# Performance work log

Measured on AMD Instinct MI355X. Metric: run time of the kernel, lower is better.

## Reference

```python
import jax, jax.numpy as jnp
import numpy as np
import math

B, N, D_IN, D_V, H, D_FF = 8, 2048, 256, 256, 8, 512
HD = D_V // H  # head dim = 32
EPS = 1e-5


def layernorm(x, g, b):
    mu = jnp.mean(x, axis=-1, keepdims=True)
    var = jnp.mean(jnp.square(x - mu), axis=-1, keepdims=True)
    return (x - mu) * jax.lax.rsqrt(var + EPS) * g + b


def setup_inputs() -> dict:
    key = jax.random.key(0)
    ks = jax.random.split(key, 12)
    s = 1.0 / math.sqrt(D_IN)
    return {
        "x": jax.random.normal(ks[0], (B, N, D_IN), jnp.float32),
        "y": jax.random.normal(ks[1], (B, N, D_IN), jnp.float32),
        "Wq": jax.random.normal(ks[2], (D_IN, D_V), jnp.float32) * s,
        "bq": jnp.zeros((D_V,), jnp.float32),
        "Wk": jax.random.normal(ks[3], (D_IN, D_V), jnp.float32) * s,
        "bk": jnp.zeros((D_V,), jnp.float32),
        "Wv": jax.random.normal(ks[4], (D_IN, D_V), jnp.float32) * s,
        "bv": jnp.zeros((D_V,), jnp.float32),
        "W1": jax.random.normal(ks[5], (D_V, D_FF), jnp.float32) * s,
        "b1": jnp.zeros((D_FF,), jnp.float32),
        "W2": jax.random.normal(ks[6], (D_FF, D_V), jnp.float32) * (1.0 / math.sqrt(D_FF)),
        "b2": jnp.zeros((D_V,), jnp.float32),
        "ln0_g": jnp.ones((D_IN,), jnp.float32),
        "ln0_b": jnp.zeros((D_IN,), jnp.float32),
        "ln1_g": jnp.ones((D_V,), jnp.float32),
        "ln1_b": jnp.zeros((D_V,), jnp.float32),
    }


def reference(x, y, Wq, bq, Wk, bk, Wv, bv, W1, b1, W2, b2, ln0_g, ln0_b, ln1_g, ln1_b):
    xn = layernorm(x, ln0_g, ln0_b)                      # ln0 on queries
    Q = (xn @ Wq + bq).reshape(B, N, H, HD)              # [B,Nq,H,hd]
    K = (y @ Wk + bk).reshape(B, N, H, HD)
    V = (y @ Wv + bv).reshape(B, N, H, HD)
    # NOTE: faithful scale = 1/sqrt(dim_V) (full model dim), not head dim
    S = jnp.einsum("bqhd,bkhd->bhqk", Q, K) / math.sqrt(D_V)
    A = jax.nn.softmax(S, axis=-1)
    O = Q + jnp.einsum("bhqk,bkhd->bqhd", A, V)          # per-head residual Q_ + A
    O = O.reshape(B, N, D_V)
    On = layernorm(O, ln1_g, ln1_b)
    ff = jax.nn.gelu(On @ W1 + b1, approximate=False) @ W2 + b2
    return O + ff
```

## Files before the change

kernel.cpp:

```cpp
#include <hip/hip_runtime.h>
#include <math.h>

#define RTOT 16384
#define NSEQ 2048
#define NHEAD 8
#define HDIM 32
#define QSCALE 0.09017132252479462f

typedef __attribute__((ext_vector_type(8))) short short8;
typedef __attribute__((ext_vector_type(4))) float f32x4;

#define GLOBAL_AS(p) ((__attribute__((address_space(1))) void*)(p))
#define LDS_AS(p) ((__attribute__((address_space(3))) void*)(p))

__device__ __forceinline__ unsigned pack_bf16(float a, float b) {
  unsigned ua = __float_as_uint(a) + 0x8000u;
  unsigned ub = __float_as_uint(b) + 0x8000u;
  return (ua >> 16) | (ub & 0xffff0000u);
}
__device__ __forceinline__ ushort bf16_1(float a) {
  return (ushort)((__float_as_uint(a) + 0x8000u) >> 16);
}

__global__ __launch_bounds__(256) void stage0_kernel(
    const float* __restrict__ x, const float* __restrict__ y,
    const float* __restrict__ Wq, const float* __restrict__ Wk,
    const float* __restrict__ Wv, const float* __restrict__ W1,
    const float* __restrict__ W2, const float* __restrict__ ln0g,
    const float* __restrict__ ln0b, ushort* __restrict__ Wqt,
    ushort* __restrict__ Wkt, ushort* __restrict__ Wvt,
    ushort* __restrict__ W1t, ushort* __restrict__ W2t,
    ushort* __restrict__ yh, ushort* __restrict__ xh) {
  const int bid = blockIdx.x;
  const int t = threadIdx.x;
  if (bid < 112) {
    const float* W;
    ushort* Wt;
    int K, N, tile;
    if (bid < 16) { W = Wq; Wt = Wqt; K = 256; N = 256; tile = bid; }
    else if (bid < 32) { W = Wk; Wt = Wkt; K = 256; N = 256; tile = bid - 16; }
    else if (bid < 48) { W = Wv; Wt = Wvt; K = 256; N = 256; tile = bid - 32; }
    else if (bid < 80) { W = W1; Wt = W1t; K = 256; N = 512; tile = bid - 48; }
    else { W = W2; Wt = W2t; K = 512; N = 256; tile = bid - 80; }
    const int tn = N >> 6;
    const int k0 = (tile / tn) << 6, n0 = (tile % tn) << 6;
    __shared__ float T[64][65];
#pragma unroll
    for (int i = 0; i < 16; ++i) {
      const int idx = t + i * 256;
      const int r = idx >> 6, c = idx & 63;
      T[r][c] = W[(size_t)(k0 + r) * N + n0 + c];
    }
    __syncthreads();
#pragma unroll
    for (int i = 0; i < 16; ++i) {
      const int idx = t + i * 256;
      const int r = idx >> 6, c = idx & 63;
      Wt[(size_t)(n0 + r) * K + k0 + c] = bf16_1(T[c][r]);
    }
  } else if (bid < 4208) {
    const size_t i = ((size_t)(bid - 112) * 256 + t) * 4;
    const float4 v = *(const float4*)&y[i];
    uint2 pk;
    pk.x = pack_bf16(v.x, v.y);
    pk.y = pack_bf16(v.z, v.w);
    *(uint2*)&yh[i] = pk;
  } else {
    const int lane = t & 63, wave = t >> 6;
    const size_t row = (size_t)(bid - 4208) * 4 + wave;
    const float* xr = x + row * 256;
    float4 v = *(const float4*)&xr[lane * 4];
    float s = v.x + v.y + v.z + v.w;
#pragma unroll
    for (int m = 1; m < 64; m <<= 1) s += __shfl_xor(s, m, 64);
    const float mu = s * (1.0f / 256.0f);
    const float dx = v.x - mu, dy = v.y - mu, dz = v.z - mu, dw = v.w - mu;
    float ss = dx * dx + dy * dy + dz * dz + dw * dw;
#pragma unroll
    for (int m = 1; m < 64; m <<= 1) ss += __shfl_xor(ss, m, 64);
    const float rstd = rsqrtf(ss * (1.0f / 256.0f) + 1e-5f);
    const float4 gv = *(const float4*)&ln0g[lane * 4];
    const float4 bv = *(const float4*)&ln0b[lane * 4];
    uint2 pk;
    pk.x = pack_bf16(dx * rstd * gv.x + bv.x, dy * rstd * gv.y + bv.y);
    pk.y = pack_bf16(dz * rstd * gv.z + bv.z, dw * rstd * gv.w + bv.w);
    *(uint2*)&xh[row * 256 + lane * 4] = pk;
  }
}

__global__ __launch_bounds__(256) void ln_kernel(
    const float* __restrict__ X, const float* __restrict__ g,
    const float* __restrict__ bt, ushort* __restrict__ Yh) {
  const int lane = threadIdx.x & 63;
  const int wave = threadIdx.x >> 6;
  const size_t row = (size_t)blockIdx.x * 4 + wave;
  const float* xr = X + row * 256;
  float4 v = *(const float4*)&xr[lane * 4];
  float s = v.x + v.y + v.z + v.w;
#pragma unroll
  for (int m = 1; m < 64; m <<= 1) s += __shfl_xor(s, m, 64);
  const float mu = s * (1.0f / 256.0f);
  const float dx = v.x - mu, dy = v.y - mu, dz = v.z - mu, dw = v.w - mu;
  float ss = dx * dx + dy * dy + dz * dz + dw * dw;
#pragma unroll
  for (int m = 1; m < 64; m <<= 1) ss += __shfl_xor(ss, m, 64);
  const float rstd = rsqrtf(ss * (1.0f / 256.0f) + 1e-5f);
  const float4 gv = *(const float4*)&g[lane * 4];
  const float4 bv = *(const float4*)&bt[lane * 4];
  uint2 pk;
  pk.x = pack_bf16(dx * rstd * gv.x + bv.x, dy * rstd * gv.y + bv.y);
  pk.y = pack_bf16(dz * rstd * gv.z + bv.z, dw * rstd * gv.w + bv.w);
  *(uint2*)&Yh[row * 256 + lane * 4] = pk;
}

__global__ __launch_bounds__(256) void qkv_kernel(
    const ushort* __restrict__ xh, const ushort* __restrict__ yh,
    const ushort* __restrict__ Wqt, const ushort* __restrict__ Wkt,
    const ushort* __restrict__ Wvt, const float* __restrict__ bq,
    const float* __restrict__ bk, const float* __restrict__ bv,
    float* __restrict__ Qf, ushort* __restrict__ Qh,
    ushort* __restrict__ Kh, ushort* __restrict__ VhT) {
  __shared__ union UU {
    struct { ushort As[128 * 32]; ushort Bs[64 * 32]; } s;
    ushort Ct[64 * 136];
  } u;
  const int t = threadIdx.x;
  const int lane = t & 63, wave = t >> 6;
  const int l16 = lane & 15, quad = lane >> 4;
  const int row0 = blockIdx.x * 128;
  const int ny = blockIdx.y;
  const int which = ny >> 2;
  const int n0 = (ny & 3) << 6;
  const ushort* A = (which == 2) ? xh : yh;
  const ushort* W = (which == 0) ? Wkt : (which == 1) ? Wvt : Wqt;
  const float* bs = (which == 0) ? bk : (which == 1) ? bv : bq;
  const int mrow = (wave & 1) * 64, ncol = (wave >> 1) * 32;

  const ushort* gA0 = A + (size_t)(row0 + (t >> 2)) * 256 + ((t & 3) << 3);
  const ushort* gA1 = gA0 + (size_t)64 * 256;
  const ushort* gB = W + (size_t)(n0 + (t >> 2)) * 256 + ((t & 3) << 3);
  ushort* lA0 = u.s.As + 8 * t;
  ushort* lA1 = u.s.As + 2048 + 8 * t;
  ushort* lB = u.s.Bs + 8 * t;

  f32x4 acc[4][2] = {};
  for (int kc = 0; kc < 256; kc += 32) {
    __builtin_amdgcn_global_load_lds(GLOBAL_AS(gA0 + kc), LDS_AS(lA0), 16, 0, 0);
    __builtin_amdgcn_global_load_lds(GLOBAL_AS(gA1 + kc), LDS_AS(lA1), 16, 0, 0);
    __builtin_amdgcn_global_load_lds(GLOBAL_AS(gB + kc), LDS_AS(lB), 16, 0, 0);
    __syncthreads();
    short8 af[4], bfr[2];
#pragma unroll
    for (int mi = 0; mi < 4; ++mi)
      af[mi] = *(const short8*)&u.s.As[(mrow + mi * 16 + l16) * 32 + quad * 8];
#pragma unroll
    for (int nj = 0; nj < 2; ++nj)
      bfr[nj] = *(const short8*)&u.s.Bs[(ncol + nj * 16 + l16) * 32 + quad * 8];
#pragma unroll
    for (int mi = 0; mi < 4; ++mi)
#pragma unroll
      for (int nj = 0; nj < 2; ++nj)
        acc[mi][nj] = __builtin_amdgcn_mfma_f32_16x16x32_bf16(
            af[mi], bfr[nj], acc[mi][nj], 0, 0, 0);
    __syncthreads();
  }

  if (which == 1) {
#pragma unroll
    for (int nj = 0; nj < 2; ++nj) {
      const int nloc = ncol + nj * 16 + l16;
      const float bvv = bs[n0 + nloc];
#pragma unroll
      for (int mi = 0; mi < 4; ++mi)
#pragma unroll
        for (int r = 0; r < 4; ++r)
          u.Ct[nloc * 136 + mrow + mi * 16 + quad * 4 + r] =
              bf16_1(acc[mi][nj][r] + bvv);
    }
    __syncthreads();
    const int bb = row0 >> 11, ns0 = row0 & 2047;
#pragma unroll
    for (int i = 0; i < 4; ++i) {
      const int c = t + i * 256;
      const int rr = c >> 4, c8 = (c & 15) << 3;
      *(float4*)&VhT[(size_t)(bb * 256 + n0 + rr) * 2048 + ns0 + c8] =
          *(const float4*)&u.Ct[rr * 136 + c8];
    }
  } else {
#pragma unroll
    for (int nj = 0; nj < 2; ++nj) {
      const int n = n0 + ncol + nj * 16 + l16;
      const float bvv = bs[n];
#pragma unroll
      for (int mi = 0; mi < 4; ++mi) {
#pragma unroll
        for (int r = 0; r < 4; ++r) {
          const size_t m = (size_t)row0 + mrow + mi * 16 + quad * 4 + r;
          const float v = acc[mi][nj][r] + bvv;
          if (which == 2) {
            Qf[m * 256 + n] = v;
            Qh[m * 256 + n] = bf16_1(v * QSCALE);
          } else {
            Kh[m * 256 + n] = bf16_1(v);
          }
        }
      }
    }
  }
}

template <int MODE>
__global__ __launch_bounds__(256) void mgemm_kernel(
    const ushort* __restrict__ A, const ushort* __restrict__ Wt,
    const float* __restrict__ bias, const float* __restrict__ res,
    float* __restrict__ Cf, ushort* __restrict__ Ch, int K, int N) {
  __shared__ ushort As[128 * 32];
  __shared__ ushort Bs[64 * 32];
  const int t = threadIdx.x;
  const int lane = t & 63, wave = t >> 6;
  const int l16 = lane & 15, quad = lane >> 4;
  const int row0 = blockIdx.x * 128;
  const int n0 = blockIdx.y << 6;
  const int mrow = (wave & 1) * 64, ncol = (wave >> 1) * 32;

  const ushort* gA0 = A + (size_t)(row0 + (t >> 2)) * K + ((t & 3) << 3);
  const ushort* gA1 = gA0 + (size_t)64 * K;
  const ushort* gB = Wt + (size_t)(n0 + (t >> 2)) * K + ((t & 3) << 3);
  ushort* lA0 = As + 8 * t;
  ushort* lA1 = As + 2048 + 8 * t;
  ushort* lB = Bs + 8 * t;

  f32x4 acc[4][2] = {};
  for (int kc = 0; kc < K; kc += 32) {
    __builtin_amdgcn_global_load_lds(GLOBAL_AS(gA0 + kc), LDS_AS(lA0), 16, 0, 0);
    __builtin_amdgcn_global_load_lds(GLOBAL_AS(gA1 + kc), LDS_AS(lA1), 16, 0, 0);
    __builtin_amdgcn_global_load_lds(GLOBAL_AS(gB + kc), LDS_AS(lB), 16, 0, 0);
    __syncthreads();
    short8 af[4], bfr[2];
#pragma unroll
    for (int mi = 0; mi < 4; ++mi)
      af[mi] = *(const short8*)&As[(mrow + mi * 16 + l16) * 32 + quad * 8];
#pragma unroll
    for (int nj = 0; nj < 2; ++nj)
      bfr[nj] = *(const short8*)&Bs[(ncol + nj * 16 + l16) * 32 + quad * 8];
#pragma unroll
    for (int mi = 0; mi < 4; ++mi)
#pragma unroll
      for (int nj = 0; nj < 2; ++nj)
        acc[mi][nj] = __builtin_amdgcn_mfma_f32_16x16x32_bf16(
            af[mi], bfr[nj], acc[mi][nj], 0, 0, 0);
    __syncthreads();
  }
#pragma unroll
  for (int nj = 0; nj < 2; ++nj) {
    const int n = n0 + ncol + nj * 16 + l16;
    const float bvv = bias[n];
#pragma unroll
    for (int mi = 0; mi < 4; ++mi) {
#pragma unroll
      for (int r = 0; r < 4; ++r) {
        const size_t m = (size_t)row0 + mrow + mi * 16 + quad * 4 + r;
        float v = acc[mi][nj][r] + bvv;
        if (MODE == 2) {
          v = 0.5f * v * (1.0f + erff(v * 0.70710678118654752f));
          Ch[m * N + n] = bf16_1(v);
        }
        if (MODE == 3) Cf[m * N + n] = v + res[m * N + n];
      }
    }
  }
}

__global__ __launch_bounds__(256) void attn_kernel(
    const float* __restrict__ Qf, const ushort* __restrict__ Qh,
    const ushort* __restrict__ Kh, const ushort* __restrict__ VhT,
    float* __restrict__ O) {
  __shared__ ushort Ks[2][64][40];
  __shared__ ushort Vt[2][32][72];
  __shared__ ushort Pl[4][16][72];

  const int t = threadIdx.x;
  const int lane = t & 63, wave = t >> 6;
  const int l16 = lane & 15, quad = lane >> 4;
  const int bh = blockIdx.x & 63;
  const int qt = blockIdx.x >> 6;
  const int b = bh >> 3, h = bh & 7;

  const size_t rowQ = (size_t)(b * NSEQ + qt * 64 + wave * 16 + l16);
  const short8 qfrag = *(const short8*)&Qh[rowQ * 256 + h * HDIM + quad * 8];
  const short8 ones = {16256, 16256, 16256, 16256,
                       16256, 16256, 16256, 16256};
  const f32x4 cinit = {-8.f, -8.f, -8.f, -8.f};

  f32x4 oacc0 = {0.f, 0.f, 0.f, 0.f}, oacc1 = {0.f, 0.f, 0.f, 0.f};
  f32x4 oaccS = {0.f, 0.f, 0.f, 0.f};

  const int kr = t >> 2, kc8 = (t & 3) << 3;
  const int vd = t >> 3, vc8 = (t & 7) << 3;
  const ushort* gK = Kh + ((size_t)(b * NSEQ + kr)) * 256 + h * HDIM + kc8;
  const ushort* gV = VhT + ((size_t)(bh * 32 + vd)) * 2048 + vc8;

  float4 kreg = *(const float4*)gK;
  float4 vreg = *(const float4*)gV;

  for (int kt = 0; kt < 32; ++kt) {
    const int bf = kt & 1;
    *(float4*)&Ks[bf][kr][kc8] = kreg;
    *(float4*)&Vt[bf][vd][vc8] = vreg;
    __syncthreads();
    if (kt < 31) {
      kreg = *(const float4*)(gK + (size_t)(kt + 1) * 64 * 256);
      vreg = *(const float4*)(gV + (kt + 1) * 64);
    }

    f32x4 sa[4];
#pragma unroll
    for (int sub = 0; sub < 4; ++sub) {
      const short8 kf = *(const short8*)&Ks[bf][sub * 16 + l16][quad * 8];
      sa[sub] = __builtin_amdgcn_mfma_f32_16x16x32_bf16(kf, qfrag, cinit, 0, 0, 0);
    }
#pragma unroll
    for (int sub = 0; sub < 4; ++sub) {
      float p0 = __builtin_amdgcn_exp2f(sa[sub][0]);
      float p1 = __builtin_amdgcn_exp2f(sa[sub][1]);
      float p2 = __builtin_amdgcn_exp2f(sa[sub][2]);
      float p3 = __builtin_amdgcn_exp2f(sa[sub][3]);
      uint2 pk;
      pk.x = pack_bf16(p0, p1);
      pk.y = pack_bf16(p2, p3);
      *(uint2*)&Pl[wave][l16][sub * 16 + quad * 4] = pk;
    }
    __threadfence_block();

    const short8 pf0 = *(const short8*)&Pl[wave][l16][quad * 8];
    const short8 pf1 = *(const short8*)&Pl[wave][l16][32 + quad * 8];
    const short8 vf00 = *(const short8*)&Vt[bf][l16][quad * 8];
    const short8 vf01 = *(const short8*)&Vt[bf][l16][32 + quad * 8];
    const short8 vf10 = *(const short8*)&Vt[bf][16 + l16][quad * 8];
    const short8 vf11 = *(const short8*)&Vt[bf][16 + l16][32 + quad * 8];
    oacc0 = __builtin_amdgcn_mfma_f32_16x16x32_bf16(pf0, vf00, oacc0, 0, 0, 0);
    oacc0 = __builtin_amdgcn_mfma_f32_16x16x32_bf16(pf1, vf01, oacc0, 0, 0, 0);
    oacc1 = __builtin_amdgcn_mfma_f32_16x16x32_bf16(pf0, vf10, oacc1, 0, 0, 0);
    oacc1 = __builtin_amdgcn_mfma_f32_16x16x32_bf16(pf1, vf11, oacc1, 0, 0, 0);
    oaccS = __builtin_amdgcn_mfma_f32_16x16x32_bf16(pf0, ones, oaccS, 0, 0, 0);
    oaccS = __builtin_amdgcn_mfma_f32_16x16x32_bf16(pf1, ones, oaccS, 0, 0, 0);
  }

  const size_t row0 = (size_t)(b * NSEQ + qt * 64 + wave * 16 + quad * 4);
#pragma unroll
  for (int r = 0; r < 4; ++r) {
    const float il = 1.0f / oaccS[r];
    const size_t ro = (row0 + r) * 256 + h * HDIM + l16;
    O[ro] = Qf[ro] + oacc0[r] * il;
    O[ro + 16] = Qf[ro + 16] + oacc1[r] * il;
  }
}

extern "C" void kernel_launch(void* const* d_in, const int* in_sizes, int n_in,
                              void* d_out, int out_size, void* d_ws, size_t ws_size,
                              hipStream_t stream) {
  const float* x = (const float*)d_in[0];
  const float* y = (const float*)d_in[1];
  const float* Wq = (const float*)d_in[2];
  const float* bq = (const float*)d_in[3];
  const float* Wk = (const float*)d_in[4];
  const float* bk = (const float*)d_in[5];
  const float* Wv = (const float*)d_in[6];
  const float* bv = (const float*)d_in[7];
  const float* W1 = (const float*)d_in[8];
  const float* b1 = (const float*)d_in[9];
  const float* W2 = (const float*)d_in[10];
  const float* b2 = (const float*)d_in[11];
  const float* ln0g = (const float*)d_in[12];
  const float* ln0b = (const float*)d_in[13];
  const float* ln1g = (const float*)d_in[14];
  const float* ln1b = (const float*)d_in[15];
  float* out = (float*)d_out;
  char* base = (char*)d_ws;

  const size_t RM = (size_t)RTOT * 256;
  ushort* yh = (ushort*)base;
  float* Ob = (float*)base;
  float* Qf = (float*)(base + RM * 4);
  ushort* Qh = (ushort*)(base + 2 * RM * 4);
  ushort* Kh = (ushort*)(base + 2 * RM * 4 + RM * 2);
  ushort* VhT = (ushort*)(base + 3 * RM * 4);
  ushort* xh = (ushort*)(base + 3 * RM * 4 + RM * 2);
  ushort* Onh = xh;
  ushort* Hidh = Qh;
  char* wbase = base + 4 * RM * 4;
  ushort* Wqt = (ushort*)wbase;
  ushort* Wkt = Wqt + 65536;
  ushort* Wvt = Wkt + 65536;
  ushort* W1t = Wvt + 65536;
  ushort* W2t = W1t + 131072;

  stage0_kernel<<<8304, 256, 0, stream>>>(x, y, Wq, Wk, Wv, W1, W2, ln0g, ln0b,
                                          Wqt, Wkt, Wvt, W1t, W2t, yh, xh);
  qkv_kernel<<<dim3(128, 12), 256, 0, stream>>>(xh, yh, Wqt, Wkt, Wvt, bq, bk,
                                                bv, Qf, Qh, Kh, VhT);
  attn_kernel<<<2048, 256, 0, stream>>>(Qf, Qh, Kh, VhT, Ob);
  ln_kernel<<<RTOT / 4, 256, 0, stream>>>(Ob, ln1g, ln1b, Onh);
  mgemm_kernel<2><<<dim3(128, 8), 256, 0, stream>>>(Onh, W1t, b1, nullptr,
                                                    nullptr, Hidh, 256, 512);
  mgemm_kernel<3><<<dim3(128, 4), 256, 0, stream>>>(Hidh, W2t, b2, Ob, out,
                                                    nullptr, 512, 256);
}
```

Baseline: 235.0 us.

## Load K fragments directly from global into registers, skipping LDS staging in attention

The attention kernel no longer stages K tiles through shared memory. Each wave loads its own K MFMA fragments straight from global into a double-buffered register set, prefetched one tile ahead. This removes LDS writes and reads for K but has all four waves load the same K data, raising global/L2 traffic and register use. It also switches the P bf16 packing to truncation instead of rounding and sets a min-blocks-per-CU launch bound of 4.

```diff
diff --git a/kernel.cpp b/kernel.cpp
--- a/kernel.cpp
+++ b/kernel.cpp
@@ -17,6 +17,9 @@
   unsigned ua = __float_as_uint(a) + 0x8000u;
   unsigned ub = __float_as_uint(b) + 0x8000u;
   return (ua >> 16) | (ub & 0xffff0000u);
+}
+__device__ __forceinline__ unsigned pack_bf16_trunc(float a, float b) {
+  return (__float_as_uint(a) >> 16) | (__float_as_uint(b) & 0xffff0000u);
 }
 __device__ __forceinline__ ushort bf16_1(float a) {
   return (ushort)((__float_as_uint(a) + 0x8000u) >> 16);
@@ -271,11 +274,10 @@
   }
 }
 
-__global__ __launch_bounds__(256) void attn_kernel(
+__global__ __launch_bounds__(256, 4) void attn_kernel(
     const float* __restrict__ Qf, const ushort* __restrict__ Qh,
     const ushort* __restrict__ Kh, const ushort* __restrict__ VhT,
     float* __restrict__ O) {
-  __shared__ ushort Ks[2][64][40];
   __shared__ ushort Vt[2][32][72];
   __shared__ ushort Pl[4][16][72];
 
@@ -295,30 +297,33 @@
   f32x4 oacc0 = {0.f, 0.f, 0.f, 0.f}, oacc1 = {0.f, 0.f, 0.f, 0.f};
   f32x4 oaccS = {0.f, 0.f, 0.f, 0.f};
 
-  const int kr = t >> 2, kc8 = (t & 3) << 3;
+  const ushort* gK = Kh + ((size_t)(b * NSEQ) + l16) * 256 + h * HDIM + quad * 8;
   const int vd = t >> 3, vc8 = (t & 7) << 3;
-  const ushort* gK = Kh + ((size_t)(b * NSEQ + kr)) * 256 + h * HDIM + kc8;
-  const ushort* gV = VhT + ((size_t)(bh * 32 + vd)) * 2048 + vc8;
-
-  float4 kreg = *(const float4*)gK;
+  const ushort* gV = VhT + ((size_t)(bh * 32) + vd) * 2048 + vc8;
+
+  short8 kcur[4], knxt[4];
+#pragma unroll
+  for (int sub = 0; sub < 4; ++sub)
+    kcur[sub] = *(const short8*)(gK + (size_t)(sub * 16) * 256);
   float4 vreg = *(const float4*)gV;
 
   for (int kt = 0; kt < 32; ++kt) {
     const int bf = kt & 1;
-    *(float4*)&Ks[bf][kr][kc8] = kreg;
     *(float4*)&Vt[bf][vd][vc8] = vreg;
     __syncthreads();
     if (kt < 31) {
-      kreg = *(const float4*)(gK + (size_t)(kt + 1) * 64 * 256);
       vreg = *(const float4*)(gV + (kt + 1) * 64);
+#pragma unroll
+      for (int sub = 0; sub < 4; ++sub)
+        knxt[sub] =
+            *(const short8*)(gK + (size_t)((kt + 1) * 64 + sub * 16) * 256);
     }
 
     f32x4 sa[4];
 #pragma unroll
-    for (int sub = 0; sub < 4; ++sub) {
-      const short8 kf = *(const short8*)&Ks[bf][sub * 16 + l16][quad * 8];
-      sa[sub] = __builtin_amdgcn_mfma_f32_16x16x32_bf16(kf, qfrag, cinit, 0, 0, 0);
-    }
+    for (int sub = 0; sub < 4; ++sub)
+      sa[sub] =
+          __builtin_amdgcn_mfma_f32_16x16x32_bf16(kcur[sub], qfrag, cinit, 0, 0, 0);
 #pragma unroll
     for (int sub = 0; sub < 4; ++sub) {
       float p0 = __builtin_amdgcn_exp2f(sa[sub][0]);
@@ -326,8 +331,8 @@
       float p2 = __builtin_amdgcn_exp2f(sa[sub][2]);
       float p3 = __builtin_amdgcn_exp2f(sa[sub][3]);
       uint2 pk;
-      pk.x = pack_bf16(p0, p1);
-      pk.y = pack_bf16(p2, p3);
+      pk.x = pack_bf16_trunc(p0, p1);
+      pk.y = pack_bf16_trunc(p2, p3);
       *(uint2*)&Pl[wave][l16][sub * 16 + quad * 4] = pk;
     }
     __threadfence_block();
@@ -344,6 +349,9 @@
     oacc1 = __builtin_amdgcn_mfma_f32_16x16x32_bf16(pf1, vf11, oacc1, 0, 0, 0);
     oaccS = __builtin_amdgcn_mfma_f32_16x16x32_bf16(pf0, ones, oaccS, 0, 0, 0);
     oaccS = __builtin_amdgcn_mfma_f32_16x16x32_bf16(pf1, ones, oaccS, 0, 0, 0);
+
+#pragma unroll
+    for (int sub = 0; sub < 4; ++sub) kcur[sub] = knxt[sub];
   }
 
   const size_t row0 = (size_t)(b * NSEQ + qt * 64 + wave * 16 + quad * 4);
```

Result: slower. 304.7 us (+29.7%).

## Process two query tiles per wave in attention and drop fp32 Q buffer

Applied to the files above, without the earlier changes.

Each attention wave now handles 32 query rows instead of 16, reusing every K/V tile loaded into LDS for twice the queries, and the grid is halved. The fp32 Q copy is no longer written by the QKV kernel or read by attention; the residual Q is reconstructed from the scaled bf16 Q, which removes a full fp32 write and read pass. P is packed with truncation instead of rounding, saving a few ALU ops. The trade-off is lower precision in the residual term and probabilities, plus higher register use per wave.

```diff
diff --git a/kernel.cpp b/kernel.cpp
--- a/kernel.cpp
+++ b/kernel.cpp
@@ -6,6 +6,7 @@
 #define NHEAD 8
 #define HDIM 32
 #define QSCALE 0.09017132252479462f
+#define QINV (1.0f / QSCALE)
 
 typedef __attribute__((ext_vector_type(8))) short short8;
 typedef __attribute__((ext_vector_type(4))) float f32x4;
@@ -18,8 +19,14 @@
   unsigned ub = __float_as_uint(b) + 0x8000u;
   return (ua >> 16) | (ub & 0xffff0000u);
 }
+__device__ __forceinline__ unsigned pack_bf16_trunc(float a, float b) {
+  return (__float_as_uint(a) >> 16) | (__float_as_uint(b) & 0xffff0000u);
+}
 __device__ __forceinline__ ushort bf16_1(float a) {
   return (ushort)((__float_as_uint(a) + 0x8000u) >> 16);
+}
+__device__ __forceinline__ float bf16_to_f(ushort u) {
+  return __uint_as_float(((unsigned)u) << 16);
 }
 
 __global__ __launch_bounds__(256) void stage0_kernel(
@@ -118,8 +125,8 @@
     const ushort* __restrict__ Wqt, const ushort* __restrict__ Wkt,
     const ushort* __restrict__ Wvt, const float* __restrict__ bq,
     const float* __restrict__ bk, const float* __restrict__ bv,
-    float* __restrict__ Qf, ushort* __restrict__ Qh,
-    ushort* __restrict__ Kh, ushort* __restrict__ VhT) {
+    ushort* __restrict__ Qh, ushort* __restrict__ Kh,
+    ushort* __restrict__ VhT) {
   __shared__ union UU {
     struct { ushort As[128 * 32]; ushort Bs[64 * 32]; } s;
     ushort Ct[64 * 136];
@@ -197,12 +204,8 @@
         for (int r = 0; r < 4; ++r) {
           const size_t m = (size_t)row0 + mrow + mi * 16 + quad * 4 + r;
           const float v = acc[mi][nj][r] + bvv;
-          if (which == 2) {
-            Qf[m * 256 + n] = v;
-            Qh[m * 256 + n] = bf16_1(v * QSCALE);
-          } else {
-            Kh[m * 256 + n] = bf16_1(v);
-          }
+          if (which == 2) Qh[m * 256 + n] = bf16_1(v * QSCALE);
+          else Kh[m * 256 + n] = bf16_1(v);
         }
       }
     }
@@ -272,12 +275,11 @@
 }
 
 __global__ __launch_bounds__(256) void attn_kernel(
-    const float* __restrict__ Qf, const ushort* __restrict__ Qh,
-    const ushort* __restrict__ Kh, const ushort* __restrict__ VhT,
-    float* __restrict__ O) {
+    const ushort* __restrict__ Qh, const ushort* __restrict__ Kh,
+    const ushort* __restrict__ VhT, float* __restrict__ O) {
   __shared__ ushort Ks[2][64][40];
   __shared__ ushort Vt[2][32][72];
-  __shared__ ushort Pl[4][16][72];
+  __shared__ ushort Pl[4][2][16][72];
 
   const int t = threadIdx.x;
   const int lane = t & 63, wave = t >> 6;
@@ -286,14 +288,17 @@
   const int qt = blockIdx.x >> 6;
   const int b = bh >> 3, h = bh & 7;
 
-  const size_t rowQ = (size_t)(b * NSEQ + qt * 64 + wave * 16 + l16);
-  const short8 qfrag = *(const short8*)&Qh[rowQ * 256 + h * HDIM + quad * 8];
+  const size_t rowQ0 = (size_t)(b * NSEQ + qt * 128 + wave * 32 + l16);
+  const short8 qfrag0 = *(const short8*)&Qh[rowQ0 * 256 + h * HDIM + quad * 8];
+  const short8 qfrag1 =
+      *(const short8*)&Qh[(rowQ0 + 16) * 256 + h * HDIM + quad * 8];
   const short8 ones = {16256, 16256, 16256, 16256,
                        16256, 16256, 16256, 16256};
   const f32x4 cinit = {-8.f, -8.f, -8.f, -8.f};
 
-  f32x4 oacc0 = {0.f, 0.f, 0.f, 0.f}, oacc1 = {0.f, 0.f, 0.f, 0.f};
-  f32x4 oaccS = {0.f, 0.f, 0.f, 0.f};
+  f32x4 o00 = {0.f, 0.f, 0.f, 0.f}, o01 = {0.f, 0.f, 0.f, 0.f};
+  f32x4 o10 = {0.f, 0.f, 0.f, 0.f}, o11 = {0.f, 0.f, 0.f, 0.f};
+  f32x4 s0 = {0.f, 0.f, 0.f, 0.f}, s1 = {0.f, 0.f, 0.f, 0.f};
 
   const int kr = t >> 2, kc8 = (t & 3) << 3;
   const int vd = t >> 3, vc8 = (t & 7) << 3;
@@ -313,46 +318,91 @@
       vreg = *(const float4*)(gV + (kt + 1) * 64);
     }
 
-    f32x4 sa[4];
-#pragma unroll
-    for (int sub = 0; sub < 4; ++sub) {
-      const short8 kf = *(const short8*)&Ks[bf][sub * 16 + l16][quad * 8];
-      sa[sub] = __builtin_amdgcn_mfma_f32_16x16x32_bf16(kf, qfrag, cinit, 0, 0, 0);
-    }
-#pragma unroll
-    for (int sub = 0; sub < 4; ++sub) {
-      float p0 = __builtin_amdgcn_exp2f(sa[sub][0]);
-      float p1 = __builtin_amdgcn_exp2f(sa[sub][1]);
-      float p2 = __builtin_amdgcn_exp2f(sa[sub][2]);
-      float p3 = __builtin_amdgcn_exp2f(sa[sub][3]);
-      uint2 pk;
-      pk.x = pack_bf16(p0, p1);
-      pk.y = pack_bf16(p2, p3);
-      *(uint2*)&Pl[wave][l16][sub * 16 + quad * 4] = pk;
-    }
-    __threadfence_block();
-
-    const short8 pf0 = *(const short8*)&Pl[wave][l16][quad * 8];
-    const short8 pf1 = *(const short8*)&Pl[wave][l16][32 + quad * 8];
+    short8 kf[4];
+#pragma unroll
+    for (int sub = 0; sub < 4; ++sub)
+      kf[sub] = *(const short8*)&Ks[bf][sub * 16 + l16][quad * 8];
     const short8 vf00 = *(const short8*)&Vt[bf][l16][quad * 8];
     const short8 vf01 = *(const short8*)&Vt[bf][l16][32 + quad * 8];
     const short8 vf10 = *(const short8*)&Vt[bf][16 + l16][quad * 8];
     const short8 vf11 = *(const short8*)&Vt[bf][16 + l16][32 + quad * 8];
-    oacc0 = __builtin_amdgcn_mfma_f32_16x16x32_bf16(pf0, vf00, oacc0, 0, 0, 0);
-    oacc0 = __builtin_amdgcn_mfma_f32_16x16x32_bf16(pf1, vf01, oacc0, 0, 0, 0);
-    oacc1 = __builtin_amdgcn_mfma_f32_16x16x32_bf16(pf0, vf10, oacc1, 0, 0, 0);
-    oacc1 = __builtin_amdgcn_mfma_f32_16x16x32_bf16(pf1, vf11, oacc1, 0, 0, 0);
-    oaccS = __builtin_amdgcn_mfma_f32_16x16x32_bf16(pf0, ones, oaccS, 0, 0, 0);
-    oaccS = __builtin_amdgcn_mfma_f32_16x16x32_bf16(pf1, ones, oaccS, 0, 0, 0);
-  }
-
-  const size_t row0 = (size_t)(b * NSEQ + qt * 64 + wave * 16 + quad * 4);
-#pragma unroll
-  for (int r = 0; r < 4; ++r) {
-    const float il = 1.0f / oaccS[r];
-    const size_t ro = (row0 + r) * 256 + h * HDIM + l16;
-    O[ro] = Qf[ro] + oacc0[r] * il;
-    O[ro + 16] = Qf[ro + 16] + oacc1[r] * il;
+
+    {
+      f32x4 sa[4];
+#pragma unroll
+      for (int sub = 0; sub < 4; ++sub)
+        sa[sub] = __builtin_amdgcn_mfma_f32_16x16x32_bf16(kf[sub], qfrag0,
+                                                          cinit, 0, 0, 0);
+#pragma unroll
+      for (int sub = 0; sub < 4; ++sub) {
+        float p0 = __builtin_amdgcn_exp2f(sa[sub][0]);
+        float p1 = __builtin_amdgcn_exp2f(sa[sub][1]);
+        float p2 = __builtin_amdgcn_exp2f(sa[sub][2]);
+        float p3 = __builtin_amdgcn_exp2f(sa[sub][3]);
+        uint2 pk;
+        pk.x = pack_bf16_trunc(p0, p1);
+        pk.y = pack_bf16_trunc(p2, p3);
+        *(uint2*)&Pl[wave][0][l16][sub * 16 + quad * 4] = pk;
+      }
+      __threadfence_block();
+      const short8 pf0 = *(const short8*)&Pl[wave][0][l16][quad * 8];
+      const short8 pf1 = *(const short8*)&Pl[wave][0][l16][32 + quad * 8];
+      o00 = __builtin_amdgcn_mfma_f32_16x16x32_bf16(pf0, vf00, o00, 0, 0, 0);
+      o00 = __builtin_amdgcn_mfma_f32_16x16x32_bf16(pf1, vf01, o00, 0, 0, 0);
+      o01 = __builtin_amdgcn_mfma_f32_16x16x32_bf16(pf0, vf10, o01, 0, 0, 0);
+      o01 = __builtin_amdgcn_mfma_f32_16x16x32_bf16(pf1, vf11, o01, 0, 0, 0);
+      s0 = __builtin_amdgcn_mfma_f32_16x16x32_bf16(pf0, ones, s0, 0, 0, 0);
+      s0 = __builtin_amdgcn_mfma_f32_16x16x32_bf16(pf1, ones, s0, 0, 0, 0);
+    }
+    {
+      f32x4 sa[4];
+#pragma unroll
+      for (int sub = 0; sub < 4; ++sub)
+        sa[sub] = __builtin_amdgcn_mfma_f32_16x16x32_bf16(kf[sub], qfrag1,
+                                                          cinit, 0, 0, 0);
+#pragma unroll
+      for (int sub = 0; sub < 4; ++sub) {
+        float p0 = __builtin_amdgcn_exp2f(sa[sub][0]);
+        float p1 = __builtin_amdgcn_exp2f(sa[sub][1]);
+        float p2 = __builtin_amdgcn_exp2f(sa[sub][2]);
+        float p3 = __builtin_amdgcn_exp2f(sa[sub][3]);
+        uint2 pk;
+        pk.x = pack_bf16_trunc(p0, p1);
+        pk.y = pack_bf16_trunc(p2, p3);
+        *(uint2*)&Pl[wave][1][l16][sub * 16 + quad * 4] = pk;
+      }
+      __threadfence_block();
+      const short8 pf0 = *(const short8*)&Pl[wave][1][l16][quad * 8];
+      const short8 pf1 = *(const short8*)&Pl[wave][1][l16][32 + quad * 8];
+      o10 = __builtin_amdgcn_mfma_f32_16x16x32_bf16(pf0, vf00, o10, 0, 0, 0);
+      o10 = __builtin_amdgcn_mfma_f32_16x16x32_bf16(pf1, vf01, o10, 0, 0, 0);
+      o11 = __builtin_amdgcn_mfma_f32_16x16x32_bf16(pf0, vf10, o11, 0, 0, 0);
+      o11 = __builtin_amdgcn_mfma_f32_16x16x32_bf16(pf1, vf11, o11, 0, 0, 0);
+      s1 = __builtin_amdgcn_mfma_f32_16x16x32_bf16(pf0, ones, s1, 0, 0, 0);
+      s1 = __builtin_amdgcn_mfma_f32_16x16x32_bf16(pf1, ones, s1, 0, 0, 0);
+    }
+  }
+
+  __threadfence_block();
+  *(short8*)&Pl[wave][0][l16][quad * 8] = qfrag0;
+  *(short8*)&Pl[wave][1][l16][quad * 8] = qfrag1;
+  __threadfence_block();
+#pragma unroll
+  for (int g = 0; g < 2; ++g) {
+    const f32x4 oS = g ? s1 : s0;
+    const f32x4 oa = g ? o10 : o00;
+    const f32x4 ob = g ? o11 : o01;
+    const size_t row0 =
+        (size_t)(b * NSEQ + qt * 128 + wave * 32 + g * 16 + quad * 4);
+#pragma unroll
+    for (int r = 0; r < 4; ++r) {
+      const float q0 = bf16_to_f(Pl[wave][g][quad * 4 + r][l16]) * QINV;
+      const float q1 = bf16_to_f(Pl[wave][g][quad * 4 + r][16 + l16]) * QINV;
+      const float il = 1.0f / oS[r];
+      const size_t ro = (row0 + r) * 256 + h * HDIM + l16;
+      O[ro] = q0 + oa[r] * il;
+      O[ro + 16] = q1 + ob[r] * il;
+    }
   }
 }
 
@@ -381,7 +431,6 @@
   const size_t RM = (size_t)RTOT * 256;
   ushort* yh = (ushort*)base;
   float* Ob = (float*)base;
-  float* Qf = (float*)(base + RM * 4);
   ushort* Qh = (ushort*)(base + 2 * RM * 4);
   ushort* Kh = (ushort*)(base + 2 * RM * 4 + RM * 2);
   ushort* VhT = (ushort*)(base + 3 * RM * 4);
@@ -398,8 +447,8 @@
   stage0_kernel<<<8304, 256, 0, stream>>>(x, y, Wq, Wk, Wv, W1, W2, ln0g, ln0b,
                                           Wqt, Wkt, Wvt, W1t, W2t, yh, xh);
   qkv_kernel<<<dim3(128, 12), 256, 0, stream>>>(xh, yh, Wqt, Wkt, Wvt, bq, bk,
-                                                bv, Qf, Qh, Kh, VhT);
-  attn_kernel<<<2048, 256, 0, stream>>>(Qf, Qh, Kh, VhT, Ob);
+                                                bv, Qh, Kh, VhT);
+  attn_kernel<<<1024, 256, 0, stream>>>(Qh, Kh, VhT, Ob);
   ln_kernel<<<RTOT / 4, 256, 0, stream>>>(Ob, ln1g, ln1b, Onh);
   mgemm_kernel<2><<<dim3(128, 8), 256, 0, stream>>>(Onh, W1t, b1, nullptr,
                                                     nullptr, Hidh, 256, 512);
```

Result: faster. 226.5 us (-3.6%).
